# Kernel optimization log

Hardware: AMD Instinct MI355X
Metric: run time of the kernel (lower is better)

## Reference

```python
import jax, jax.numpy as jnp
import numpy as np

N, M, P, H = 200000, 20, 64, 256
EPS = 1e-12  # inside sqrt: avoids NaN grads when duplicate neighbors give zero distance


def setup_inputs() -> dict:
    key = jax.random.key(0)
    ks = jax.random.split(key, 8)
    x = jax.random.normal(ks[0], (N, P), jnp.float32)
    pos = jax.random.uniform(ks[1], (N, 2), jnp.float32) * 10.0
    y = jax.random.normal(ks[2], (N,), jnp.float32)
    # m distinct-from-self neighbor indices per node (offset trick avoids self loops)
    off = jax.random.randint(ks[3], (N, M), 1, N)
    nbr_idx = ((jnp.arange(N)[:, None] + off) % N).astype(jnp.int32)
    theta = jnp.array([1.0, 1.0, 0.1], jnp.float32)  # (sigma_sq, phi, tau)
    w1 = jax.random.normal(ks[4], (P, H), jnp.float32) * (1.0 / np.sqrt(P))
    b1 = jnp.zeros((H,), jnp.float32)
    w2 = jax.random.normal(ks[5], (H, 1), jnp.float32) * (1.0 / np.sqrt(H))
    b2 = jnp.zeros((1,), jnp.float32)
    return dict(x=x, pos=pos, y=y, nbr_idx=nbr_idx, theta=theta,
                w1=w1, b1=b1, w2=w2, b2=b2)


def _dist(a, b):
    return jnp.sqrt(jnp.sum((a - b) ** 2, axis=-1) + EPS)


def reference(x, pos, y, nbr_idx, theta, w1, b1, w2, b2):
    sigma_sq, phi, tau = theta[0], theta[1], theta[2]
    tau_sq = tau * sigma_sq
    m = nbr_idx.shape[1]
    pos_nbr = pos[nbr_idx]                                            # [N,M,2] gather
    # Cov(i, N(i)): exponential covariance of node-to-neighbor distances  [N,M]
    cov_i_ni = sigma_sq * jnp.exp(-phi * _dist(pos[:, None, :], pos_nbr))
    # Cov(N(i), N(i)) + nugget on the diagonal                          [N,M,M]
    d_nn = _dist(pos_nbr[:, :, None, :], pos_nbr[:, None, :, :])
    cov = sigma_sq * jnp.exp(-phi * d_nn) + tau_sq * jnp.eye(m, dtype=pos.dtype)
    # B_i = Cov(N,N)^{-1} Cov(i,N)  (batched small solve == inv @ vec)  [N,M]
    b_i = jnp.linalg.solve(cov, cov_i_ni[..., None])[..., 0]
    f_i = sigma_sq + tau - jnp.sum(b_i * cov_i_ni, axis=1)             # [N]
    inv_sqrt_f = 1.0 / jnp.sqrt(f_i)
    # MLP: Linear -> ReLU -> Linear, squeezed to [N]
    o = (jax.nn.relu(x @ w1 + b1) @ w2 + b2)[:, 0]
    y_decor = (y - jnp.sum(y[nbr_idx] * b_i, axis=1)) * inv_sqrt_f
    o_decor = (o - jnp.sum(o[nbr_idx] * b_i, axis=1)) * inv_sqrt_f
    return (y_decor, o_decor, o)
```

## Files before the change

kernel.cpp:

```cpp
#include <hip/hip_runtime.h>


#define MM   20
#define PP   64
#define HH   256
#define EPSF 1e-12f
#define WSTR 24

#define CSE(j, r) csx[2*(j)*((j)+1) + (r)]
#define C20(r)    csx[60 + (r)]

typedef __attribute__((ext_vector_type(8))) short bf16x8;
typedef __attribute__((ext_vector_type(4))) float f32x4;

static __device__ __forceinline__ unsigned short f2bf(float f) {
    unsigned int u = __builtin_bit_cast(unsigned int, f);
    u += 0x7fffu + ((u >> 16) & 1u);
    return (unsigned short)(u >> 16);
}
static __device__ __forceinline__ float bf2f(unsigned short h) {
    unsigned int u = ((unsigned int)h) << 16;
    return __builtin_bit_cast(float, u);
}

#define QSWZ(v, pat) __builtin_bit_cast(float, __builtin_amdgcn_ds_swizzle( \
    __builtin_bit_cast(int, (v)), 0x8000 | (pat)))

#define GATH(R) mall[R] = QSWZ(mv[(R) >> 2], 0x55 * ((R) & 3));

#define SCASE(K, P) case K: {                                              \
    _Pragma("unroll")                                                      \
    for (int j = (P); j < 5; ++j) pk[j] = CSE(j, (K));                     \
    p20 = C20(K);                                                          \
    pd  = QSWZ(pk[(P)], 0x55 * ((K) & 3));                                 \
} break;

#define BSTEP(R, JMIN) {                                                   \
    float acc = 0.0f;                                                      \
    _Pragma("unroll")                                                      \
    for (int j = (JMIN); j < 5; ++j) {                                     \
        float t = CSE(j, (R)) * bl[j];                                     \
        acc += (4*j + h_ > (R)) ? t : 0.0f;                                \
    }                                                                      \
    acc += __shfl_xor(acc, 1, 64);                                         \
    acc += __shfl_xor(acc, 2, 64);                                         \
    float pdr = QSWZ(CSE((R) >> 2, (R)), 0x55 * ((R) & 3));                \
    float rr = __builtin_amdgcn_rcpf(pdr);                                 \
    rr = rr * (2.0f - pdr * rr);                                           \
    float bR = (C20(R) - acc) * rr;                                        \
    if (((R) & 3) == h_) bl[(R) >> 2] = bR;                                \
}

__global__ __launch_bounds__(256, 2)
void fused_kernel(const float* __restrict__ x,
                  const float* __restrict__ w1,
                  const float* __restrict__ b1,
                  const float* __restrict__ w2,
                  const float* __restrict__ b2,
                  const float* __restrict__ pos,
                  const int*   __restrict__ nbr,
                  const float* __restrict__ theta,
                  float* __restrict__ o_out,
                  float* __restrict__ wis,
                  int n, int nm)
{
    __shared__ __align__(16) short swh[PP * HH];
    __shared__ __align__(16) short swl[PP * HH];
    __shared__ float sb1[HH];
    __shared__ float sw2[HH];

    const int b   = blockIdx.x;
    const int grp = b / 3;
    const int rem = b - grp * 3;
    const int tid = threadIdx.x;

    if (rem == 1 && grp < nm) {
        {
            const int col = tid;
            const int t = col >> 4, nn = col & 15;
            #pragma unroll
            for (int g = 0; g < 8; ++g) {
                const int s = g >> 2, q = g & 3;
                bf16x8 hv, lv;
                #pragma unroll
                for (int u = 0; u < 8; ++u) {
                    float v = w1[(g * 8 + u) * HH + col];
                    unsigned short h = f2bf(v);
                    hv[u] = (short)h;
                    lv[u] = (short)f2bf(v - bf2f(h));
                }
                const int base = ((((t * 2 + s) * 4 + q) * 16) + nn) * 8;
                *(bf16x8*)&swh[base] = hv;
                *(bf16x8*)&swl[base] = lv;
            }
            sb1[tid] = b1[tid];
            sw2[tid] = w2[tid];
        }
        __syncthreads();

        const int lane = tid & 63;
        const int wv   = tid >> 6;
        const int nn   = lane & 15;
        const int q    = lane >> 4;
        const int wb   = grp * 128 + wv * 32;

        bf16x8 ah[2][2], al[2][2];
        #pragma unroll
        for (int mt = 0; mt < 2; ++mt) {
            const int row = wb + mt * 16 + nn;
            #pragma unroll
            for (int s = 0; s < 2; ++s) {
                float v[8];
                if (row < n) {
                    const float* xp = x + (size_t)row * PP + s * 32 + q * 8;
                    float4 va = *(const float4*)(xp);
                    float4 vb = *(const float4*)(xp + 4);
                    v[0]=va.x; v[1]=va.y; v[2]=va.z; v[3]=va.w;
                    v[4]=vb.x; v[5]=vb.y; v[6]=vb.z; v[7]=vb.w;
                } else {
                    #pragma unroll
                    for (int u = 0; u < 8; ++u) v[u] = 0.0f;
                }
                bf16x8 h, l;
                #pragma unroll
                for (int u = 0; u < 8; ++u) {
                    unsigned short hb = f2bf(v[u]);
                    h[u] = (short)hb;
                    l[u] = (short)f2bf(v[u] - bf2f(hb));
                }
                ah[mt][s] = h;
                al[mt][s] = l;
            }
        }

        float part[2][4];
        #pragma unroll
        for (int mt = 0; mt < 2; ++mt)
            #pragma unroll
            for (int r = 0; r < 4; ++r) part[mt][r] = 0.0f;

        #pragma unroll
        for (int t = 0; t < 16; ++t) {
            f32x4 acc[2];
            #pragma unroll
            for (int mt = 0; mt < 2; ++mt) acc[mt] = (f32x4)(0.0f);
            #pragma unroll
            for (int s = 0; s < 2; ++s) {
                const int fb = ((((t * 2 + s) * 4 + q) * 16) + nn) * 8;
                bf16x8 bh = *(const bf16x8*)&swh[fb];
                bf16x8 bl2 = *(const bf16x8*)&swl[fb];
                #pragma unroll
                for (int mt = 0; mt < 2; ++mt) {
                    acc[mt] = __builtin_amdgcn_mfma_f32_16x16x32_bf16(ah[mt][s], bh,  acc[mt], 0, 0, 0);
                    acc[mt] = __builtin_amdgcn_mfma_f32_16x16x32_bf16(al[mt][s], bh,  acc[mt], 0, 0, 0);
                    acc[mt] = __builtin_amdgcn_mfma_f32_16x16x32_bf16(ah[mt][s], bl2, acc[mt], 0, 0, 0);
                }
            }
            const float b1t = sb1[t * 16 + nn];
            const float w2t = sw2[t * 16 + nn];
            #pragma unroll
            for (int mt = 0; mt < 2; ++mt)
                #pragma unroll
                for (int r = 0; r < 4; ++r)
                    part[mt][r] = fmaf(fmaxf(acc[mt][r] + b1t, 0.0f), w2t, part[mt][r]);
        }

        #pragma unroll
        for (int w = 1; w < 16; w <<= 1)
            #pragma unroll
            for (int mt = 0; mt < 2; ++mt)
                #pragma unroll
                for (int r = 0; r < 4; ++r)
                    part[mt][r] += __shfl_xor(part[mt][r], w, 64);

        const float bb = b2[0];
        if (nn == 0) {
            #pragma unroll
            for (int mt = 0; mt < 2; ++mt) {
                const int row = wb + mt * 16 + q * 4;
                if (row < n) {
                    float4 o4 = make_float4(part[mt][0] + bb, part[mt][1] + bb,
                                            part[mt][2] + bb, part[mt][3] + bb);
                    *(float4*)&o_out[row] = o4;
                }
            }
        }
        return;
    }

    {
        int mcnt = (b + 1) / 3; if (mcnt > nm) mcnt = nm;
        const int sidx = b - mcnt;
        const int h_   = tid & 3;
        const int i    = sidx * 64 + (tid >> 2);
        if (i >= n) return;

        const float sigma_sq = theta[0];
        const float phi      = theta[1];
        const float tau      = theta[2];
        const float tau_sq   = tau * sigma_sq;

        const float L2E = 1.44269504088896340736f;
        const float c1  = -phi * L2E;
        const float c0  = __builtin_amdgcn_logf(sigma_sq);

        const float sqrtEPS = __builtin_amdgcn_sqrtf(EPSF);
        const float diagA   = __builtin_amdgcn_exp2f(fmaf(sqrtEPS, c1, c0)) + tau_sq;
        const float diagB   = sigma_sq + tau;

        int idx[MM];
        const int4* nb4 = (const int4*)(nbr + (size_t)i * MM);
        #pragma unroll
        for (int k = 0; k < MM / 4; ++k) {
            int4 v = nb4[k];
            idx[4*k] = v.x; idx[4*k+1] = v.y; idx[4*k+2] = v.z; idx[4*k+3] = v.w;
        }

        float px[21], py[21];
        const float2* pos2 = (const float2*)pos;
        #pragma unroll
        for (int j = 0; j < MM; ++j) {
            float2 p = pos2[idx[j]];
            px[j] = p.x; py[j] = p.y;
        }
        {
            float2 p = pos2[i];
            px[20] = p.x; py[20] = p.y;
        }

        float cx[5], cy[5];
        #pragma unroll
        for (int j = 0; j < 5; ++j) {
            int cj = nbr[(size_t)i * MM + 4*j + h_];
            float2 p = pos2[cj];
            cx[j] = p.x; cy[j] = p.y;
        }

        float csx[81];
        #pragma unroll
        for (int j = 0; j < 5; ++j) {
            #pragma unroll
            for (int r = 0; r <= 4*j + 3; ++r) {
                float dx = px[r] - cx[j];
                float dy = py[r] - cy[j];
                float d  = __builtin_amdgcn_sqrtf(fmaf(dx, dx, fmaf(dy, dy, EPSF)));
                float v  = __builtin_amdgcn_exp2f(fmaf(d, c1, c0));
                v = (r == 4*j + h_) ? diagA : v;
                CSE(j, r) = v;
            }
        }
        #pragma unroll
        for (int r = 0; r < 20; ++r) {
            float dx = px[r] - px[20];
            float dy = py[r] - py[20];
            float d  = __builtin_amdgcn_sqrtf(fmaf(dx, dx, fmaf(dy, dy, EPSF)));
            C20(r)   = __builtin_amdgcn_exp2f(fmaf(d, c1, c0));
        }
        C20(20) = diagB;

        float pk[5], mv[5], mall[21], p20, pd;

        #pragma unroll 1
        for (int k = 0; k < 4; ++k) {
            switch (k) {
            SCASE(0,0) SCASE(1,0) SCASE(2,0) SCASE(3,0)
            default: break;
            }
            float rp = __builtin_amdgcn_rcpf(pd);
            rp = rp * (2.0f - pd * rp);
            #pragma unroll
            for (int j = 0; j < 5; ++j)
                mv[j] = (4*j + h_ > k) ? pk[j] * rp : 0.0f;
            GATH(0)  GATH(1)  GATH(2)  GATH(3)  GATH(4)  GATH(5)  GATH(6)
            GATH(7)  GATH(8)  GATH(9)  GATH(10) GATH(11) GATH(12) GATH(13)
            GATH(14) GATH(15) GATH(16) GATH(17) GATH(18) GATH(19)
            mall[20] = p20 * rp;
            #pragma unroll
            for (int j = 0; j < 5; ++j) {
                float pkj = pk[j];
                #pragma unroll
                for (int r = 0; r <= 4*j + 3; ++r)
                    CSE(j, r) = fmaf(-mall[r], pkj, CSE(j, r));
            }
            #pragma unroll
            for (int r = 0; r <= 20; ++r)
                C20(r) = fmaf(-mall[r], p20, C20(r));
        }

        #pragma unroll 1
        for (int k = 4; k < 8; ++k) {
            switch (k) {
            SCASE(4,1) SCASE(5,1) SCASE(6,1) SCASE(7,1)
            default: break;
            }
            float rp = __builtin_amdgcn_rcpf(pd);
            rp = rp * (2.0f - pd * rp);
            #pragma unroll
            for (int j = 1; j < 5; ++j)
                mv[j] = (4*j + h_ > k) ? pk[j] * rp : 0.0f;
            GATH(4)  GATH(5)  GATH(6)  GATH(7)  GATH(8)  GATH(9)  GATH(10)
            GATH(11) GATH(12) GATH(13) GATH(14) GATH(15) GATH(16) GATH(17)
            GATH(18) GATH(19)
            mall[20] = p20 * rp;
            #pragma unroll
            for (int j = 1; j < 5; ++j) {
                float pkj = pk[j];
                #pragma unroll
                for (int r = 4; r <= 4*j + 3; ++r)
                    CSE(j, r) = fmaf(-mall[r], pkj, CSE(j, r));
            }
            #pragma unroll
            for (int r = 4; r <= 20; ++r)
                C20(r) = fmaf(-mall[r], p20, C20(r));
        }

        #pragma unroll 1
        for (int k = 8; k < 12; ++k) {
            switch (k) {
            SCASE(8,2) SCASE(9,2) SCASE(10,2) SCASE(11,2)
            default: break;
            }
            float rp = __builtin_amdgcn_rcpf(pd);
            rp = rp * (2.0f - pd * rp);
            #pragma unroll
            for (int j = 2; j < 5; ++j)
                mv[j] = (4*j + h_ > k) ? pk[j] * rp : 0.0f;
            GATH(8)  GATH(9)  GATH(10) GATH(11) GATH(12) GATH(13) GATH(14)
            GATH(15) GATH(16) GATH(17) GATH(18) GATH(19)
            mall[20] = p20 * rp;
            #pragma unroll
            for (int j = 2; j < 5; ++j) {
                float pkj = pk[j];
                #pragma unroll
                for (int r = 8; r <= 4*j + 3; ++r)
                    CSE(j, r) = fmaf(-mall[r], pkj, CSE(j, r));
            }
            #pragma unroll
            for (int r = 8; r <= 20; ++r)
                C20(r) = fmaf(-mall[r], p20, C20(r));
        }

        #pragma unroll 1
        for (int k = 12; k < 16; ++k) {
            switch (k) {
            SCASE(12,3) SCASE(13,3) SCASE(14,3) SCASE(15,3)
            default: break;
            }
            float rp = __builtin_amdgcn_rcpf(pd);
            rp = rp * (2.0f - pd * rp);
            #pragma unroll
            for (int j = 3; j < 5; ++j)
                mv[j] = (4*j + h_ > k) ? pk[j] * rp : 0.0f;
            GATH(12) GATH(13) GATH(14) GATH(15) GATH(16) GATH(17) GATH(18)
            GATH(19)
            mall[20] = p20 * rp;
            #pragma unroll
            for (int j = 3; j < 5; ++j) {
                float pkj = pk[j];
                #pragma unroll
                for (int r = 12; r <= 4*j + 3; ++r)
                    CSE(j, r) = fmaf(-mall[r], pkj, CSE(j, r));
            }
            #pragma unroll
            for (int r = 12; r <= 20; ++r)
                C20(r) = fmaf(-mall[r], p20, C20(r));
        }

        #pragma unroll 1
        for (int k = 16; k < 20; ++k) {
            switch (k) {
            SCASE(16,4) SCASE(17,4) SCASE(18,4) SCASE(19,4)
            default: break;
            }
            float rp = __builtin_amdgcn_rcpf(pd);
            rp = rp * (2.0f - pd * rp);
            mv[4] = (16 + h_ > k) ? pk[4] * rp : 0.0f;
            GATH(16) GATH(17) GATH(18) GATH(19)
            mall[20] = p20 * rp;
            {
                float pkj = pk[4];
                #pragma unroll
                for (int r = 16; r <= 19; ++r)
                    CSE(4, r) = fmaf(-mall[r], pkj, CSE(4, r));
            }
            #pragma unroll
            for (int r = 16; r <= 20; ++r)
                C20(r) = fmaf(-mall[r], p20, C20(r));
        }

        float bl[5];
        BSTEP(19,5) BSTEP(18,4) BSTEP(17,4) BSTEP(16,4)
        BSTEP(15,4) BSTEP(14,3) BSTEP(13,3) BSTEP(12,3)
        BSTEP(11,3) BSTEP(10,2) BSTEP(9,2)  BSTEP(8,2)
        BSTEP(7,2)  BSTEP(6,1)  BSTEP(5,1)  BSTEP(4,1)
        BSTEP(3,1)  BSTEP(2,0)  BSTEP(1,0)  BSTEP(0,0)

        float f  = C20(20);
        float is = __builtin_amdgcn_rsqf(f);
        is = is * fmaf(-0.5f * f * is, is, 1.5f);

        float* wp = wis + (size_t)i * WSTR;
        #pragma unroll
        for (int j = 0; j < 5; ++j)
            wp[4*j + h_] = bl[j] * is;
        if (h_ == 0) wp[20] = is;
    }
}

__global__ __launch_bounds__(256, 4)
void epilogue_kernel(const int*   __restrict__ nbr,
                     const float* __restrict__ y,
                     const float* __restrict__ o_in,
                     const float* __restrict__ wis,
                     float* __restrict__ yd,
                     float* __restrict__ od, int n)
{
    const int i = blockIdx.x * 256 + threadIdx.x;
    if (i >= n) return;

    float wv_[20];
    {
        const float4* w4 = (const float4*)(wis + (size_t)i * WSTR);
        *(float4*)&wv_[0]  = w4[0];
        *(float4*)&wv_[4]  = w4[1];
        *(float4*)&wv_[8]  = w4[2];
        *(float4*)&wv_[12] = w4[3];
        *(float4*)&wv_[16] = w4[4];
    }
    const float is = wis[(size_t)i * WSTR + 20];

    int idx[MM];
    const int4* nb4 = (const int4*)(nbr + (size_t)i * MM);
    #pragma unroll
    for (int k = 0; k < MM / 4; ++k) {
        int4 v = nb4[k];
        idx[4*k] = v.x; idx[4*k+1] = v.y; idx[4*k+2] = v.z; idx[4*k+3] = v.w;
    }

    float sy = 0.0f, so = 0.0f;
    #pragma unroll
    for (int j = 0; j < MM; ++j) {
        sy = fmaf(wv_[j], y[idx[j]],    sy);
        so = fmaf(wv_[j], o_in[idx[j]], so);
    }
    yd[i] = fmaf(is, y[i],    -sy);
    od[i] = fmaf(is, o_in[i], -so);
}

extern "C" void kernel_launch(void* const* d_in, const int* in_sizes, int n_in,
                              void* d_out, int out_size, void* d_ws, size_t ws_size,
                              hipStream_t stream)
{
    const float* x     = (const float*)d_in[0];
    const float* pos   = (const float*)d_in[1];
    const float* y     = (const float*)d_in[2];
    const int*   nbr   = (const int*)  d_in[3];
    const float* theta = (const float*)d_in[4];
    const float* w1    = (const float*)d_in[5];
    const float* b1    = (const float*)d_in[6];
    const float* w2    = (const float*)d_in[7];
    const float* b2    = (const float*)d_in[8];

    const int n = in_sizes[2];
    float* out = (float*)d_out;
    float* yd = out;
    float* od = out + (size_t)n;
    float* oo = out + 2 * (size_t)n;
    float* wis = (float*)d_ws;

    const int nm = (n + 127) / 128;
    const int ns = (n + 63) / 64;
    fused_kernel<<<nm + ns, 256, 0, stream>>>(x, w1, b1, w2, b2,
                                              pos, nbr, theta, oo, wis, n, nm);
    epilogue_kernel<<<(n + 255) / 256, 256, 0, stream>>>(nbr, y, oo, wis,
                                                         yd, od, n);
}
```

Baseline: 228.7 us.

## Fuse y decorrelation into solver kernel and split epilogue across four lanes

```diff
diff --git a/kernel.cpp b/kernel.cpp
--- a/kernel.cpp
+++ b/kernel.cpp
@@ -60,8 +60,10 @@
                   const float* __restrict__ pos,
                   const int*   __restrict__ nbr,
                   const float* __restrict__ theta,
+                  const float* __restrict__ y,
                   float* __restrict__ o_out,
                   float* __restrict__ wis,
+                  float* __restrict__ yd,
                   int n, int nm)
 {
     __shared__ __align__(16) short swh[PP * HH];
@@ -147,7 +149,7 @@
             #pragma unroll
             for (int s = 0; s < 2; ++s) {
                 const int fb = ((((t * 2 + s) * 4 + q) * 16) + nn) * 8;
-                bf16x8 bh = *(const bf16x8*)&swh[fb];
+                bf16x8 bh  = *(const bf16x8*)&swh[fb];
                 bf16x8 bl2 = *(const bf16x8*)&swl[fb];
                 #pragma unroll
                 for (int mt = 0; mt < 2; ++mt) {
@@ -403,48 +405,46 @@
         #pragma unroll
         for (int j = 0; j < 5; ++j)
             wp[4*j + h_] = bl[j] * is;
-        if (h_ == 0) wp[20] = is;
+
+        float sy = 0.0f;
+        #pragma unroll
+        for (int j = 0; j < 5; ++j) {
+            int cj = nbr[(size_t)i * MM + 4*j + h_];
+            sy = fmaf(bl[j], y[cj], sy);
+        }
+        sy += __shfl_xor(sy, 1, 64);
+        sy += __shfl_xor(sy, 2, 64);
+        if (h_ == 0) {
+            wp[20] = is;
+            yd[i]  = (y[i] - sy) * is;
+        }
     }
 }
 
 __global__ __launch_bounds__(256, 4)
-void epilogue_kernel(const int*   __restrict__ nbr,
-                     const float* __restrict__ y,
-                     const float* __restrict__ o_in,
-                     const float* __restrict__ wis,
-                     float* __restrict__ yd,
-                     float* __restrict__ od, int n)
+void epilogue_od(const int*   __restrict__ nbr,
+                 const float* __restrict__ o_in,
+                 const float* __restrict__ wis,
+                 float* __restrict__ od, int n)
 {
-    const int i = blockIdx.x * 256 + threadIdx.x;
+    const int tid = threadIdx.x;
+    const int h_  = tid & 3;
+    const int i   = blockIdx.x * 64 + (tid >> 2);
     if (i >= n) return;
 
-    float wv_[20];
-    {
-        const float4* w4 = (const float4*)(wis + (size_t)i * WSTR);
-        *(float4*)&wv_[0]  = w4[0];
-        *(float4*)&wv_[4]  = w4[1];
-        *(float4*)&wv_[8]  = w4[2];
-        *(float4*)&wv_[12] = w4[3];
-        *(float4*)&wv_[16] = w4[4];
+    const float* wp = wis + (size_t)i * WSTR;
+    float so = 0.0f;
+    #pragma unroll
+    for (int j = 0; j < 5; ++j) {
+        int cj = nbr[(size_t)i * MM + 4*j + h_];
+        so = fmaf(wp[4*j + h_], o_in[cj], so);
     }
-    const float is = wis[(size_t)i * WSTR + 20];
-
-    int idx[MM];
-    const int4* nb4 = (const int4*)(nbr + (size_t)i * MM);
-    #pragma unroll
-    for (int k = 0; k < MM / 4; ++k) {
-        int4 v = nb4[k];
-        idx[4*k] = v.x; idx[4*k+1] = v.y; idx[4*k+2] = v.z; idx[4*k+3] = v.w;
+    so += __shfl_xor(so, 1, 64);
+    so += __shfl_xor(so, 2, 64);
+    if (h_ == 0) {
+        float is = wp[20];
+        od[i] = fmaf(is, o_in[i], -so);
     }
-
-    float sy = 0.0f, so = 0.0f;
-    #pragma unroll
-    for (int j = 0; j < MM; ++j) {
-        sy = fmaf(wv_[j], y[idx[j]],    sy);
-        so = fmaf(wv_[j], o_in[idx[j]], so);
-    }
-    yd[i] = fmaf(is, y[i],    -sy);
-    od[i] = fmaf(is, o_in[i], -so);
 }
 
 extern "C" void kernel_launch(void* const* d_in, const int* in_sizes, int n_in,
@@ -471,7 +471,7 @@
     const int nm = (n + 127) / 128;
     const int ns = (n + 63) / 64;
     fused_kernel<<<nm + ns, 256, 0, stream>>>(x, w1, b1, w2, b2,
-                                              pos, nbr, theta, oo, wis, n, nm);
-    epilogue_kernel<<<(n + 255) / 256, 256, 0, stream>>>(nbr, y, oo, wis,
-                                                         yd, od, n);
-}
+                                              pos, nbr, theta, y,
+                                              oo, wis, yd, n, nm);
+    epilogue_od<<<(n + 63) / 64, 256, 0, stream>>>(nbr, oo, wis, od, n);
+}
```

New measurement: 218.6 us. 4.4% less time.
